# Kernel tuning notes

Measured on AMD Instinct MI355X. Metric: run time of the kernel, lower is better.

The kernel has to match this reference:

```python
import jax, jax.numpy as jnp
import numpy as np
import math

RANK = 2
CUTOFF = 10.0
EWALD_ALPHA = 0.3
PREFACTOR = 1.0
N_ATOMS = 100000
N_PAIRS = 2000000
BOX_L = 60.0


def _damp_factors_erfc(dr, b):
    # Ewald real-space damping factors for rank<=2 multipoles. Shape (5, P).
    u = b * dr
    erfc_u = jax.lax.erfc(u)
    exp2_u = jnp.exp(-u * u)
    u2 = u * u
    u3 = u2 * u
    u5 = u3 * u2
    u7 = u5 * u2
    p1 = jnp.zeros_like(u)
    p3 = u
    p5 = (3 * u + 2 * u3) / 3
    p7 = (15 * u + 10 * u3 + 4 * u5) / 15
    p9 = (8 * u7 + 28 * u5 + 70 * u3 + 105 * u) / 105
    pref = 2.0 / math.sqrt(math.pi)
    return jnp.stack([erfc_u + pref * p * exp2_u for p in (p1, p3, p5, p7, p9)], axis=0)


def _interaction_tensor(drVec, dampFactors, drInv):
    # Rank-2 multipole interaction tensor, shape (P, 10, 10).
    drInv2 = drInv * drInv
    drInv3 = drInv2 * drInv
    drInv5 = drInv3 * drInv2
    drVec2 = drVec * drVec
    x, y, z = drVec[:, 0], drVec[:, 1], drVec[:, 2]
    x2, y2, z2 = drVec2[:, 0], drVec2[:, 1], drVec2[:, 2]
    xy, xz, yz = x * y, x * z, y * z
    drInv7 = drInv5 * drInv2
    drInv9 = drInv7 * drInv2
    if dampFactors is not None:
        drInv = drInv * dampFactors[0]
        drInv3 = drInv3 * dampFactors[1]
        drInv5 = drInv5 * dampFactors[2]
        drInv7 = drInv7 * dampFactors[3]
        drInv9 = drInv9 * dampFactors[4]
    tx, ty, tz = -x * drInv3, -y * drInv3, -z * drInv3
    txx = 3 * x2 * drInv5 - drInv3
    txy = 3 * xy * drInv5
    txz = 3 * xz * drInv5
    tyy = 3 * y2 * drInv5 - drInv3
    tyz = 3 * yz * drInv5
    tzz = 3 * z2 * drInv5 - drInv3
    txxx = -15 * x2 * x * drInv7 + 9 * x * drInv5
    txxy = -15 * x2 * y * drInv7 + 3 * y * drInv5
    txxz = -15 * x2 * z * drInv7 + 3 * z * drInv5
    tyyy = -15 * y2 * y * drInv7 + 9 * y * drInv5
    tyyx = -15 * y2 * x * drInv7 + 3 * x * drInv5
    tyyz = -15 * y2 * z * drInv7 + 3 * z * drInv5
    tzzz = -15 * z2 * z * drInv7 + 9 * z * drInv5
    tzzx = -15 * z2 * x * drInv7 + 3 * x * drInv5
    tzzy = -15 * z2 * y * drInv7 + 3 * y * drInv5
    txyz = -15 * x * y * z * drInv7
    txxxx = 105 * x2 * x2 * drInv9 - 90 * x2 * drInv7 + 9 * drInv5
    txxxy = 105 * x2 * xy * drInv9 - 45 * xy * drInv7
    txxxz = 105 * x2 * xz * drInv9 - 45 * xz * drInv7
    txxyy = 105 * x2 * y2 * drInv9 - 15 * (x2 + y2) * drInv7 + 3 * drInv5
    txxzz = 105 * x2 * z2 * drInv9 - 15 * (x2 + z2) * drInv7 + 3 * drInv5
    txxyz = 105 * x2 * yz * drInv9 - 15 * yz * drInv7
    tyyyy = 105 * y2 * y2 * drInv9 - 90 * y2 * drInv7 + 9 * drInv5
    tyyyx = 105 * y2 * xy * drInv9 - 45 * xy * drInv7
    tyyyz = 105 * y2 * yz * drInv9 - 45 * yz * drInv7
    tyyzz = 105 * y2 * z2 * drInv9 - 15 * (y2 + z2) * drInv7 + 3 * drInv5
    tyyxz = 105 * y2 * xz * drInv9 - 15 * xz * drInv7
    tzzzz = 105 * z2 * z2 * drInv9 - 90 * z2 * drInv7 + 9 * drInv5
    tzzzx = 105 * z2 * xz * drInv9 - 45 * xz * drInv7
    tzzzy = 105 * z2 * yz * drInv9 - 45 * yz * drInv7
    tzzxy = 105 * z2 * xy * drInv9 - 15 * xy * drInv7
    rows = (drInv, -tx, -ty, -tz, txx, txy, txz, tyy, tyz, tzz,
            tx, -txx, -txy, -txz, txxx, txxy, txxz, tyyx, txyz, tzzx,
            ty, -txy, -tyy, -tyz, txxy, tyyx, txyz, tyyy, tyyz, tzzy,
            tz, -txz, -tyz, -tzz, txxz, txyz, tzzx, tyyz, tzzy, tzzz,
            txx, -txxx, -txxy, -txxz, txxxx, txxxy, txxxz, txxyy, txxyz, txxzz,
            txy, -txxy, -tyyx, -txyz, txxxy, txxyy, txxyz, tyyyx, tyyxz, tzzxy,
            txz, -txxz, -txyz, -tzzx, txxxz, txxyz, txxzz, tyyxz, tzzxy, tzzzx,
            tyy, -tyyx, -tyyy, -tyyz, txxyy, tyyyx, tyyxz, tyyyy, tyyyz, tyyzz,
            tyz, -txyz, -tyyz, -tzzy, txxyz, tyyxz, tzzxy, tyyyz, tyyzz, tzzzy,
            tzz, -tzzx, -tzzy, -tzzz, txxzz, tzzxy, tzzzx, tyyzz, tzzzy, tzzzz)
    return jnp.stack(rows, axis=-1).reshape(-1, 10, 10)


def _pack_multipoles(q, p, t):
    # [q, ux, uy, uz, Qxx, Qxy, Qxz, Qyy, Qyz, Qzz], shape (N, 10).
    cols = [q[:, None], p,
            (t[:, 0, 0] / 3)[:, None],
            ((t[:, 0, 1] + t[:, 1, 0]) / 3)[:, None],
            ((t[:, 0, 2] + t[:, 2, 0]) / 3)[:, None],
            (t[:, 1, 1] / 3)[:, None],
            ((t[:, 1, 2] + t[:, 2, 1]) / 3)[:, None],
            (t[:, 2, 2] / 3)[:, None]]
    return jnp.concatenate(cols, axis=1)


def setup_inputs() -> dict:
    key = jax.random.key(0)
    k1, k2, k3, k4, k5, k6 = jax.random.split(key, 6)
    coords = jax.random.uniform(k1, (N_ATOMS, 3), dtype=jnp.float32) * BOX_L
    box = jnp.eye(3, dtype=jnp.float32) * BOX_L
    pi = jax.random.randint(k2, (N_PAIRS,), 0, N_ATOMS)
    off = jax.random.randint(k3, (N_PAIRS,), 1, N_ATOMS)
    pj = (pi + off) % N_ATOMS  # guarantee i != j
    pairs = jnp.stack([pi, pj], axis=1).astype(jnp.int64)
    q = jax.random.normal(k4, (N_ATOMS,), dtype=jnp.float32)
    p = jax.random.normal(k5, (N_ATOMS, 3), dtype=jnp.float32)
    t = jax.random.normal(k6, (N_ATOMS, 3, 3), dtype=jnp.float32)
    return {"coords": coords, "box": box, "pairs": pairs, "q": q, "p": p, "t": t}


def reference(coords, box, pairs, q, p, t):
    box_inv = jnp.linalg.inv(box)
    dr = coords[pairs[:, 1]] - coords[pairs[:, 0]]
    # minimum-image PBC (row-vector fractional coordinates convention)
    dr_vecs = dr - jnp.round(dr @ box_inv) @ box
    dist = jnp.linalg.norm(dr_vecs, axis=1)
    mask = (dist <= CUTOFF).astype(dist.dtype)
    damps = _damp_factors_erfc(dist, EWALD_ALPHA)
    i_tensor = _interaction_tensor(dr_vecs, damps, 1.0 / dist)  # (P,10,10)
    m = _pack_multipoles(q, p, t)  # (N,10)
    ene_pairs = jnp.einsum('pa,pab,pb->p', m[pairs[:, 1]], i_tensor, m[pairs[:, 0]])
    return PREFACTOR * jnp.sum(ene_pairs * mask)
```

## Files before the change

### kernel.cpp

```cpp
#include <hip/hip_runtime.h>
#include <math.h>

#define CUTOFF2 100.0f
#define EW_ALPHA 0.3f
#define SEGS 2048
#define NT 256
#define CAP 128


__global__ __launch_bounds__(NT)
void screen_kernel(const float* __restrict__ coords,
                   const float* __restrict__ box,
                   const int2* __restrict__ pairs,
                   float4* __restrict__ list,
                   int* __restrict__ counts,
                   int n_pairs, int chunk) {
    __shared__ int lcount;
    if (threadIdx.x == 0) lcount = 0;
    __syncthreads();

    const float Lx = box[0], Ly = box[4], Lz = box[8];
    const float iLx = 1.0f / Lx, iLy = 1.0f / Ly, iLz = 1.0f / Lz;

    const int b = blockIdx.x;
    const int start = b * chunk;
    const int end = min(start + chunk, n_pairs);
    for (int idx = start + threadIdx.x; idx < end; idx += NT) {
        int2 pr = pairs[idx];
        int i = pr.x, j = pr.y;
        float dx = coords[3*j+0] - coords[3*i+0];
        float dy = coords[3*j+1] - coords[3*i+1];
        float dz = coords[3*j+2] - coords[3*i+2];
        float x = dx - rintf(dx * iLx) * Lx;
        float y = dy - rintf(dy * iLy) * Ly;
        float z = dz - rintf(dz * iLz) * Lz;
        float r2 = x*x + y*y + z*z;
        if (r2 <= CUTOFF2) {
            int slot = atomicAdd(&lcount, 1);
            if (slot < CAP)
                list[b*CAP + slot] = make_float4(x, y, z, __int_as_float(idx));
        }
    }
    __syncthreads();
    if (threadIdx.x == 0) counts[b] = min(lcount, CAP);
}

__global__ __launch_bounds__(NT)
void mp_dense_kernel(const float4* __restrict__ list,
                     const int* __restrict__ counts,
                     const int2* __restrict__ pairs,
                     const float* __restrict__ q,
                     const float* __restrict__ p,
                     const float* __restrict__ t,
                     double* __restrict__ partial) {
    const float PREF = 1.1283791670955126f;
    const int b = blockIdx.x;
    const int n = counts[b];

    double acc = 0.0;
    for (int k = threadIdx.x; k < n; k += NT) {
        float4 ent = list[b*CAP + k];
        float x = ent.x, y = ent.y, z = ent.z;
        int idx = __float_as_int(ent.w);
        int2 pr = pairs[idx];
        int i = pr.x, j = pr.y;

        float r2 = x*x + y*y + z*z;
        float r = sqrtf(r2);
        float rinv = 1.0f / r;

        float u  = EW_ALPHA * r;
        float u2 = u*u;
        float u3 = u2*u, u5 = u3*u2, u7 = u5*u2;
        float e2 = expf(-u2);
        float ec = erfcf(u);
        float d1 = ec;
        float d3 = ec + PREF * u * e2;
        float d5 = ec + PREF * ((3.0f*u + 2.0f*u3) * (1.0f/3.0f)) * e2;
        float d7 = ec + PREF * ((15.0f*u + 10.0f*u3 + 4.0f*u5) * (1.0f/15.0f)) * e2;
        float d9 = ec + PREF * ((105.0f*u + 70.0f*u3 + 28.0f*u5 + 8.0f*u7) * (1.0f/105.0f)) * e2;

        float ri2 = rinv * rinv;
        float r3i = rinv * ri2;
        float r5i = r3i * ri2;
        float r7i = r5i * ri2;
        float r9i = r7i * ri2;
        float R1 = rinv * d1;
        float R3 = r3i * d3;
        float R5 = r5i * d5;
        float R7 = r7i * d7;
        float R9 = r9i * d9;

        float x2 = x*x, y2 = y*y, z2 = z*z;
        float xy = x*y, xz = x*z, yz = y*z;

        float tx = -x * R3, ty = -y * R3, tz = -z * R3;
        float txx = 3.0f*x2*R5 - R3;
        float txy = 3.0f*xy*R5;
        float txz = 3.0f*xz*R5;
        float tyy = 3.0f*y2*R5 - R3;
        float tyz = 3.0f*yz*R5;
        float tzz = 3.0f*z2*R5 - R3;
        float txxx = x*(9.0f*R5 - 15.0f*x2*R7);
        float txxy = y*(3.0f*R5 - 15.0f*x2*R7);
        float txxz = z*(3.0f*R5 - 15.0f*x2*R7);
        float tyyy = y*(9.0f*R5 - 15.0f*y2*R7);
        float tyyx = x*(3.0f*R5 - 15.0f*y2*R7);
        float tyyz = z*(3.0f*R5 - 15.0f*y2*R7);
        float tzzz = z*(9.0f*R5 - 15.0f*z2*R7);
        float tzzx = x*(3.0f*R5 - 15.0f*z2*R7);
        float tzzy = y*(3.0f*R5 - 15.0f*z2*R7);
        float txyz = -15.0f*x*yz*R7;
        float txxxx = 105.0f*x2*x2*R9 - 90.0f*x2*R7 + 9.0f*R5;
        float txxxy = xy*(105.0f*x2*R9 - 45.0f*R7);
        float txxxz = xz*(105.0f*x2*R9 - 45.0f*R7);
        float txxyy = 105.0f*x2*y2*R9 - 15.0f*(x2+y2)*R7 + 3.0f*R5;
        float txxzz = 105.0f*x2*z2*R9 - 15.0f*(x2+z2)*R7 + 3.0f*R5;
        float txxyz = yz*(105.0f*x2*R9 - 15.0f*R7);
        float tyyyy = 105.0f*y2*y2*R9 - 90.0f*y2*R7 + 9.0f*R5;
        float tyyyx = xy*(105.0f*y2*R9 - 45.0f*R7);
        float tyyyz = yz*(105.0f*y2*R9 - 45.0f*R7);
        float tyyzz = 105.0f*y2*z2*R9 - 15.0f*(y2+z2)*R7 + 3.0f*R5;
        float tyyxz = xz*(105.0f*y2*R9 - 15.0f*R7);
        float tzzzz = 105.0f*z2*z2*R9 - 90.0f*z2*R7 + 9.0f*R5;
        float tzzzx = xz*(105.0f*z2*R9 - 45.0f*R7);
        float tzzzy = yz*(105.0f*z2*R9 - 45.0f*R7);
        float tzzxy = xy*(105.0f*z2*R9 - 15.0f*R7);

        const float* ti = t + 9*i;
        const float* tj = t + 9*j;
        float mi0 = q[i];
        float mi1 = p[3*i+0], mi2 = p[3*i+1], mi3 = p[3*i+2];
        float mi4 = ti[0] * (1.0f/3.0f);
        float mi5 = (ti[1] + ti[3]) * (1.0f/3.0f);
        float mi6 = (ti[2] + ti[6]) * (1.0f/3.0f);
        float mi7 = ti[4] * (1.0f/3.0f);
        float mi8 = (ti[5] + ti[7]) * (1.0f/3.0f);
        float mi9 = ti[8] * (1.0f/3.0f);
        float mj0 = q[j];
        float mj1 = p[3*j+0], mj2 = p[3*j+1], mj3 = p[3*j+2];
        float mj4 = tj[0] * (1.0f/3.0f);
        float mj5 = (tj[1] + tj[3]) * (1.0f/3.0f);
        float mj6 = (tj[2] + tj[6]) * (1.0f/3.0f);
        float mj7 = tj[4] * (1.0f/3.0f);
        float mj8 = (tj[5] + tj[7]) * (1.0f/3.0f);
        float mj9 = tj[8] * (1.0f/3.0f);

        float E0 = R1*mi0  - tx*mi1   - ty*mi2   - tz*mi3   + txx*mi4   + txy*mi5   + txz*mi6   + tyy*mi7   + tyz*mi8   + tzz*mi9;
        float E1 = tx*mi0  - txx*mi1  - txy*mi2  - txz*mi3  + txxx*mi4  + txxy*mi5  + txxz*mi6  + tyyx*mi7  + txyz*mi8  + tzzx*mi9;
        float E2 = ty*mi0  - txy*mi1  - tyy*mi2  - tyz*mi3  + txxy*mi4  + tyyx*mi5  + txyz*mi6  + tyyy*mi7  + tyyz*mi8  + tzzy*mi9;
        float E3 = tz*mi0  - txz*mi1  - tyz*mi2  - tzz*mi3  + txxz*mi4  + txyz*mi5  + tzzx*mi6  + tyyz*mi7  + tzzy*mi8  + tzzz*mi9;
        float E4 = txx*mi0 - txxx*mi1 - txxy*mi2 - txxz*mi3 + txxxx*mi4 + txxxy*mi5 + txxxz*mi6 + txxyy*mi7 + txxyz*mi8 + txxzz*mi9;
        float E5 = txy*mi0 - txxy*mi1 - tyyx*mi2 - txyz*mi3 + txxxy*mi4 + txxyy*mi5 + txxyz*mi6 + tyyyx*mi7 + tyyxz*mi8 + tzzxy*mi9;
        float E6 = txz*mi0 - txxz*mi1 - txyz*mi2 - tzzx*mi3 + txxxz*mi4 + txxyz*mi5 + txxzz*mi6 + tyyxz*mi7 + tzzxy*mi8 + tzzzx*mi9;
        float E7 = tyy*mi0 - tyyx*mi1 - tyyy*mi2 - tyyz*mi3 + txxyy*mi4 + tyyyx*mi5 + tyyxz*mi6 + tyyyy*mi7 + tyyyz*mi8 + tyyzz*mi9;
        float E8 = tyz*mi0 - txyz*mi1 - tyyz*mi2 - tzzy*mi3 + txxyz*mi4 + tyyxz*mi5 + tzzxy*mi6 + tyyyz*mi7 + tyyzz*mi8 + tzzzy*mi9;
        float E9 = tzz*mi0 - tzzx*mi1 - tzzy*mi2 - tzzz*mi3 + txxzz*mi4 + tzzxy*mi5 + tzzzx*mi6 + tyyzz*mi7 + tzzzy*mi8 + tzzzz*mi9;

        float e = mj0*E0 + mj1*E1 + mj2*E2 + mj3*E3 + mj4*E4
                + mj5*E5 + mj6*E6 + mj7*E7 + mj8*E8 + mj9*E9;

        acc += (double)e;
    }

    __shared__ double sdata[NT];
    int tid = threadIdx.x;
    sdata[tid] = acc;
    __syncthreads();
    for (int s = NT/2; s > 0; s >>= 1) {
        if (tid < s) sdata[tid] += sdata[tid + s];
        __syncthreads();
    }
    if (tid == 0) partial[b] = sdata[0];
}

__global__ __launch_bounds__(256)
void mp_reduce_kernel(const double* __restrict__ partial, int n, float* __restrict__ out) {
    __shared__ double sdata[256];
    int tid = threadIdx.x;
    double a = 0.0;
    for (int i = tid; i < n; i += 256) a += partial[i];
    sdata[tid] = a;
    __syncthreads();
    for (int s = 128; s > 0; s >>= 1) {
        if (tid < s) sdata[tid] += sdata[tid + s];
        __syncthreads();
    }
    if (tid == 0) out[0] = (float)sdata[0];
}

extern "C" void kernel_launch(void* const* d_in, const int* in_sizes, int n_in,
                              void* d_out, int out_size, void* d_ws, size_t ws_size,
                              hipStream_t stream) {
    const float* coords = (const float*)d_in[0];
    const float* box    = (const float*)d_in[1];
    const int2*  pairs  = (const int2*)d_in[2];
    const float* q      = (const float*)d_in[3];
    const float* p      = (const float*)d_in[4];
    const float* t      = (const float*)d_in[5];
    int n_pairs = in_sizes[2] / 2;
    int chunk = (n_pairs + SEGS - 1) / SEGS;

    char* ws = (char*)d_ws;
    int*    counts  = (int*)ws;
    float4* list    = (float4*)(ws + SEGS * sizeof(int));
    double* partial = (double*)(ws + SEGS * sizeof(int) + (size_t)SEGS * CAP * sizeof(float4));

    screen_kernel<<<SEGS, NT, 0, stream>>>(coords, box, pairs, list, counts, n_pairs, chunk);
    mp_dense_kernel<<<SEGS, NT, 0, stream>>>(list, counts, pairs, q, p, t, partial);
    mp_reduce_kernel<<<1, 256, 0, stream>>>(partial, SEGS, (float*)d_out);
}
```

Baseline: 36.99 us.

## Fuse cutoff screening and multipole energy into one kernel via shared-memory list

Merges the screening kernel and the dense energy kernel into a single kernel. Each block compacts its in-cutoff pairs (displacement plus i/j indices) into shared memory and then evaluates the energy directly. This drops one kernel launch, the global list write and read, and the second read of the pairs array. Pairs are now streamed as 64-bit words with nontemporal loads, and the per-block capacity drops from 128 to 96. The lower capacity slightly raises the risk of silently dropping pairs if a segment holds unusually many in-cutoff pairs.

```diff
diff --git a/kernel.cpp b/kernel.cpp
--- a/kernel.cpp
+++ b/kernel.cpp
@@ -5,18 +5,124 @@
 #define EW_ALPHA 0.3f
 #define SEGS 2048
 #define NT 256
-#define CAP 128
-
+#define CAP 96
+
+__device__ __forceinline__ double pair_energy(float x, float y, float z,
+                                              int i, int j,
+                                              const float* __restrict__ q,
+                                              const float* __restrict__ p,
+                                              const float* __restrict__ t) {
+    const float PREF = 1.1283791670955126f;
+    float r2 = x*x + y*y + z*z;
+    float r = sqrtf(r2);
+    float rinv = 1.0f / r;
+
+    float u  = EW_ALPHA * r;
+    float u2 = u*u;
+    float u3 = u2*u, u5 = u3*u2, u7 = u5*u2;
+    float e2 = expf(-u2);
+    float ec = erfcf(u);
+    float d1 = ec;
+    float d3 = ec + PREF * u * e2;
+    float d5 = ec + PREF * ((3.0f*u + 2.0f*u3) * (1.0f/3.0f)) * e2;
+    float d7 = ec + PREF * ((15.0f*u + 10.0f*u3 + 4.0f*u5) * (1.0f/15.0f)) * e2;
+    float d9 = ec + PREF * ((105.0f*u + 70.0f*u3 + 28.0f*u5 + 8.0f*u7) * (1.0f/105.0f)) * e2;
+
+    float ri2 = rinv * rinv;
+    float r3i = rinv * ri2;
+    float r5i = r3i * ri2;
+    float r7i = r5i * ri2;
+    float r9i = r7i * ri2;
+    float R1 = rinv * d1;
+    float R3 = r3i * d3;
+    float R5 = r5i * d5;
+    float R7 = r7i * d7;
+    float R9 = r9i * d9;
+
+    float x2 = x*x, y2 = y*y, z2 = z*z;
+    float xy = x*y, xz = x*z, yz = y*z;
+
+    float tx = -x * R3, ty = -y * R3, tz = -z * R3;
+    float txx = 3.0f*x2*R5 - R3;
+    float txy = 3.0f*xy*R5;
+    float txz = 3.0f*xz*R5;
+    float tyy = 3.0f*y2*R5 - R3;
+    float tyz = 3.0f*yz*R5;
+    float tzz = 3.0f*z2*R5 - R3;
+    float txxx = x*(9.0f*R5 - 15.0f*x2*R7);
+    float txxy = y*(3.0f*R5 - 15.0f*x2*R7);
+    float txxz = z*(3.0f*R5 - 15.0f*x2*R7);
+    float tyyy = y*(9.0f*R5 - 15.0f*y2*R7);
+    float tyyx = x*(3.0f*R5 - 15.0f*y2*R7);
+    float tyyz = z*(3.0f*R5 - 15.0f*y2*R7);
+    float tzzz = z*(9.0f*R5 - 15.0f*z2*R7);
+    float tzzx = x*(3.0f*R5 - 15.0f*z2*R7);
+    float tzzy = y*(3.0f*R5 - 15.0f*z2*R7);
+    float txyz = -15.0f*x*yz*R7;
+    float txxxx = 105.0f*x2*x2*R9 - 90.0f*x2*R7 + 9.0f*R5;
+    float txxxy = xy*(105.0f*x2*R9 - 45.0f*R7);
+    float txxxz = xz*(105.0f*x2*R9 - 45.0f*R7);
+    float txxyy = 105.0f*x2*y2*R9 - 15.0f*(x2+y2)*R7 + 3.0f*R5;
+    float txxzz = 105.0f*x2*z2*R9 - 15.0f*(x2+z2)*R7 + 3.0f*R5;
+    float txxyz = yz*(105.0f*x2*R9 - 15.0f*R7);
+    float tyyyy = 105.0f*y2*y2*R9 - 90.0f*y2*R7 + 9.0f*R5;
+    float tyyyx = xy*(105.0f*y2*R9 - 45.0f*R7);
+    float tyyyz = yz*(105.0f*y2*R9 - 45.0f*R7);
+    float tyyzz = 105.0f*y2*z2*R9 - 15.0f*(y2+z2)*R7 + 3.0f*R5;
+    float tyyxz = xz*(105.0f*y2*R9 - 15.0f*R7);
+    float tzzzz = 105.0f*z2*z2*R9 - 90.0f*z2*R7 + 9.0f*R5;
+    float tzzzx = xz*(105.0f*z2*R9 - 45.0f*R7);
+    float tzzzy = yz*(105.0f*z2*R9 - 45.0f*R7);
+    float tzzxy = xy*(105.0f*z2*R9 - 15.0f*R7);
+
+    const float* ti = t + 9*i;
+    const float* tj = t + 9*j;
+    float mi0 = q[i];
+    float mi1 = p[3*i+0], mi2 = p[3*i+1], mi3 = p[3*i+2];
+    float mi4 = ti[0] * (1.0f/3.0f);
+    float mi5 = (ti[1] + ti[3]) * (1.0f/3.0f);
+    float mi6 = (ti[2] + ti[6]) * (1.0f/3.0f);
+    float mi7 = ti[4] * (1.0f/3.0f);
+    float mi8 = (ti[5] + ti[7]) * (1.0f/3.0f);
+    float mi9 = ti[8] * (1.0f/3.0f);
+    float mj0 = q[j];
+    float mj1 = p[3*j+0], mj2 = p[3*j+1], mj3 = p[3*j+2];
+    float mj4 = tj[0] * (1.0f/3.0f);
+    float mj5 = (tj[1] + tj[3]) * (1.0f/3.0f);
+    float mj6 = (tj[2] + tj[6]) * (1.0f/3.0f);
+    float mj7 = tj[4] * (1.0f/3.0f);
+    float mj8 = (tj[5] + tj[7]) * (1.0f/3.0f);
+    float mj9 = tj[8] * (1.0f/3.0f);
+
+    float E0 = R1*mi0  - tx*mi1   - ty*mi2   - tz*mi3   + txx*mi4   + txy*mi5   + txz*mi6   + tyy*mi7   + tyz*mi8   + tzz*mi9;
+    float E1 = tx*mi0  - txx*mi1  - txy*mi2  - txz*mi3  + txxx*mi4  + txxy*mi5  + txxz*mi6  + tyyx*mi7  + txyz*mi8  + tzzx*mi9;
+    float E2 = ty*mi0  - txy*mi1  - tyy*mi2  - tyz*mi3  + txxy*mi4  + tyyx*mi5  + txyz*mi6  + tyyy*mi7  + tyyz*mi8  + tzzy*mi9;
+    float E3 = tz*mi0  - txz*mi1  - tyz*mi2  - tzz*mi3  + txxz*mi4  + txyz*mi5  + tzzx*mi6  + tyyz*mi7  + tzzy*mi8  + tzzz*mi9;
+    float E4 = txx*mi0 - txxx*mi1 - txxy*mi2 - txxz*mi3 + txxxx*mi4 + txxxy*mi5 + txxxz*mi6 + txxyy*mi7 + txxyz*mi8 + txxzz*mi9;
+    float E5 = txy*mi0 - txxy*mi1 - tyyx*mi2 - txyz*mi3 + txxxy*mi4 + txxyy*mi5 + txxyz*mi6 + tyyyx*mi7 + tyyxz*mi8 + tzzxy*mi9;
+    float E6 = txz*mi0 - txxz*mi1 - txyz*mi2 - tzzx*mi3 + txxxz*mi4 + txxyz*mi5 + txxzz*mi6 + tyyxz*mi7 + tzzxy*mi8 + tzzzx*mi9;
+    float E7 = tyy*mi0 - tyyx*mi1 - tyyy*mi2 - tyyz*mi3 + txxyy*mi4 + tyyyx*mi5 + tyyxz*mi6 + tyyyy*mi7 + tyyyz*mi8 + tyyzz*mi9;
+    float E8 = tyz*mi0 - txyz*mi1 - tyyz*mi2 - tzzy*mi3 + txxyz*mi4 + tyyxz*mi5 + tzzxy*mi6 + tyyyz*mi7 + tyyzz*mi8 + tzzzy*mi9;
+    float E9 = tzz*mi0 - tzzx*mi1 - tzzy*mi2 - tzzz*mi3 + txxzz*mi4 + tzzxy*mi5 + tzzzx*mi6 + tyyzz*mi7 + tzzzy*mi8 + tzzzz*mi9;
+
+    float e = mj0*E0 + mj1*E1 + mj2*E2 + mj3*E3 + mj4*E4
+            + mj5*E5 + mj6*E6 + mj7*E7 + mj8*E8 + mj9*E9;
+    return (double)e;
+}
 
 __global__ __launch_bounds__(NT)
-void screen_kernel(const float* __restrict__ coords,
-                   const float* __restrict__ box,
-                   const int2* __restrict__ pairs,
-                   float4* __restrict__ list,
-                   int* __restrict__ counts,
-                   int n_pairs, int chunk) {
-    __shared__ int lcount;
-    if (threadIdx.x == 0) lcount = 0;
+void mp_fused_kernel(const float* __restrict__ coords,
+                     const float* __restrict__ box,
+                     const long long* __restrict__ pairs,
+                     const float* __restrict__ q,
+                     const float* __restrict__ p,
+                     const float* __restrict__ t,
+                     double* __restrict__ partial,
+                     int n_pairs, int chunk) {
+    __shared__ float sx[CAP], sy[CAP], sz[CAP];
+    __shared__ int   si[CAP], sj[CAP];
+    __shared__ int   scount;
+    if (threadIdx.x == 0) scount = 0;
     __syncthreads();
 
     const float Lx = box[0], Ly = box[4], Lz = box[8];
@@ -25,9 +131,11 @@
     const int b = blockIdx.x;
     const int start = b * chunk;
     const int end = min(start + chunk, n_pairs);
+
     for (int idx = start + threadIdx.x; idx < end; idx += NT) {
-        int2 pr = pairs[idx];
-        int i = pr.x, j = pr.y;
+        long long v = __builtin_nontemporal_load(pairs + idx);
+        int i = (int)(v & 0xffffffffLL);
+        int j = (int)(v >> 32);
         float dx = coords[3*j+0] - coords[3*i+0];
         float dy = coords[3*j+1] - coords[3*i+1];
         float dz = coords[3*j+2] - coords[3*i+2];
@@ -36,131 +144,19 @@
         float z = dz - rintf(dz * iLz) * Lz;
         float r2 = x*x + y*y + z*z;
         if (r2 <= CUTOFF2) {
-            int slot = atomicAdd(&lcount, 1);
-            if (slot < CAP)
-                list[b*CAP + slot] = make_float4(x, y, z, __int_as_float(idx));
+            int slot = atomicAdd(&scount, 1);
+            if (slot < CAP) {
+                sx[slot] = x; sy[slot] = y; sz[slot] = z;
+                si[slot] = i; sj[slot] = j;
+            }
         }
     }
     __syncthreads();
-    if (threadIdx.x == 0) counts[b] = min(lcount, CAP);
-}
-
-__global__ __launch_bounds__(NT)
-void mp_dense_kernel(const float4* __restrict__ list,
-                     const int* __restrict__ counts,
-                     const int2* __restrict__ pairs,
-                     const float* __restrict__ q,
-                     const float* __restrict__ p,
-                     const float* __restrict__ t,
-                     double* __restrict__ partial) {
-    const float PREF = 1.1283791670955126f;
-    const int b = blockIdx.x;
-    const int n = counts[b];
-
+
+    int ns = min(scount, CAP);
     double acc = 0.0;
-    for (int k = threadIdx.x; k < n; k += NT) {
-        float4 ent = list[b*CAP + k];
-        float x = ent.x, y = ent.y, z = ent.z;
-        int idx = __float_as_int(ent.w);
-        int2 pr = pairs[idx];
-        int i = pr.x, j = pr.y;
-
-        float r2 = x*x + y*y + z*z;
-        float r = sqrtf(r2);
-        float rinv = 1.0f / r;
-
-        float u  = EW_ALPHA * r;
-        float u2 = u*u;
-        float u3 = u2*u, u5 = u3*u2, u7 = u5*u2;
-        float e2 = expf(-u2);
-        float ec = erfcf(u);
-        float d1 = ec;
-        float d3 = ec + PREF * u * e2;
-        float d5 = ec + PREF * ((3.0f*u + 2.0f*u3) * (1.0f/3.0f)) * e2;
-        float d7 = ec + PREF * ((15.0f*u + 10.0f*u3 + 4.0f*u5) * (1.0f/15.0f)) * e2;
-        float d9 = ec + PREF * ((105.0f*u + 70.0f*u3 + 28.0f*u5 + 8.0f*u7) * (1.0f/105.0f)) * e2;
-
-        float ri2 = rinv * rinv;
-        float r3i = rinv * ri2;
-        float r5i = r3i * ri2;
-        float r7i = r5i * ri2;
-        float r9i = r7i * ri2;
-        float R1 = rinv * d1;
-        float R3 = r3i * d3;
-        float R5 = r5i * d5;
-        float R7 = r7i * d7;
-        float R9 = r9i * d9;
-
-        float x2 = x*x, y2 = y*y, z2 = z*z;
-        float xy = x*y, xz = x*z, yz = y*z;
-
-        float tx = -x * R3, ty = -y * R3, tz = -z * R3;
-        float txx = 3.0f*x2*R5 - R3;
-        float txy = 3.0f*xy*R5;
-        float txz = 3.0f*xz*R5;
-        float tyy = 3.0f*y2*R5 - R3;
-        float tyz = 3.0f*yz*R5;
-        float tzz = 3.0f*z2*R5 - R3;
-        float txxx = x*(9.0f*R5 - 15.0f*x2*R7);
-        float txxy = y*(3.0f*R5 - 15.0f*x2*R7);
-        float txxz = z*(3.0f*R5 - 15.0f*x2*R7);
-        float tyyy = y*(9.0f*R5 - 15.0f*y2*R7);
-        float tyyx = x*(3.0f*R5 - 15.0f*y2*R7);
-        float tyyz = z*(3.0f*R5 - 15.0f*y2*R7);
-        float tzzz = z*(9.0f*R5 - 15.0f*z2*R7);
-        float tzzx = x*(3.0f*R5 - 15.0f*z2*R7);
-        float tzzy = y*(3.0f*R5 - 15.0f*z2*R7);
-        float txyz = -15.0f*x*yz*R7;
-        float txxxx = 105.0f*x2*x2*R9 - 90.0f*x2*R7 + 9.0f*R5;
-        float txxxy = xy*(105.0f*x2*R9 - 45.0f*R7);
-        float txxxz = xz*(105.0f*x2*R9 - 45.0f*R7);
-        float txxyy = 105.0f*x2*y2*R9 - 15.0f*(x2+y2)*R7 + 3.0f*R5;
-        float txxzz = 105.0f*x2*z2*R9 - 15.0f*(x2+z2)*R7 + 3.0f*R5;
-        float txxyz = yz*(105.0f*x2*R9 - 15.0f*R7);
-        float tyyyy = 105.0f*y2*y2*R9 - 90.0f*y2*R7 + 9.0f*R5;
-        float tyyyx = xy*(105.0f*y2*R9 - 45.0f*R7);
-        float tyyyz = yz*(105.0f*y2*R9 - 45.0f*R7);
-        float tyyzz = 105.0f*y2*z2*R9 - 15.0f*(y2+z2)*R7 + 3.0f*R5;
-        float tyyxz = xz*(105.0f*y2*R9 - 15.0f*R7);
-        float tzzzz = 105.0f*z2*z2*R9 - 90.0f*z2*R7 + 9.0f*R5;
-        float tzzzx = xz*(105.0f*z2*R9 - 45.0f*R7);
-        float tzzzy = yz*(105.0f*z2*R9 - 45.0f*R7);
-        float tzzxy = xy*(105.0f*z2*R9 - 15.0f*R7);
-
-        const float* ti = t + 9*i;
-        const float* tj = t + 9*j;
-        float mi0 = q[i];
-        float mi1 = p[3*i+0], mi2 = p[3*i+1], mi3 = p[3*i+2];
-        float mi4 = ti[0] * (1.0f/3.0f);
-        float mi5 = (ti[1] + ti[3]) * (1.0f/3.0f);
-        float mi6 = (ti[2] + ti[6]) * (1.0f/3.0f);
-        float mi7 = ti[4] * (1.0f/3.0f);
-        float mi8 = (ti[5] + ti[7]) * (1.0f/3.0f);
-        float mi9 = ti[8] * (1.0f/3.0f);
-        float mj0 = q[j];
-        float mj1 = p[3*j+0], mj2 = p[3*j+1], mj3 = p[3*j+2];
-        float mj4 = tj[0] * (1.0f/3.0f);
-        float mj5 = (tj[1] + tj[3]) * (1.0f/3.0f);
-        float mj6 = (tj[2] + tj[6]) * (1.0f/3.0f);
-        float mj7 = tj[4] * (1.0f/3.0f);
-        float mj8 = (tj[5] + tj[7]) * (1.0f/3.0f);
-        float mj9 = tj[8] * (1.0f/3.0f);
-
-        float E0 = R1*mi0  - tx*mi1   - ty*mi2   - tz*mi3   + txx*mi4   + txy*mi5   + txz*mi6   + tyy*mi7   + tyz*mi8   + tzz*mi9;
-        float E1 = tx*mi0  - txx*mi1  - txy*mi2  - txz*mi3  + txxx*mi4  + txxy*mi5  + txxz*mi6  + tyyx*mi7  + txyz*mi8  + tzzx*mi9;
-        float E2 = ty*mi0  - txy*mi1  - tyy*mi2  - tyz*mi3  + txxy*mi4  + tyyx*mi5  + txyz*mi6  + tyyy*mi7  + tyyz*mi8  + tzzy*mi9;
-        float E3 = tz*mi0  - txz*mi1  - tyz*mi2  - tzz*mi3  + txxz*mi4  + txyz*mi5  + tzzx*mi6  + tyyz*mi7  + tzzy*mi8  + tzzz*mi9;
-        float E4 = txx*mi0 - txxx*mi1 - txxy*mi2 - txxz*mi3 + txxxx*mi4 + txxxy*mi5 + txxxz*mi6 + txxyy*mi7 + txxyz*mi8 + txxzz*mi9;
-        float E5 = txy*mi0 - txxy*mi1 - tyyx*mi2 - txyz*mi3 + txxxy*mi4 + txxyy*mi5 + txxyz*mi6 + tyyyx*mi7 + tyyxz*mi8 + tzzxy*mi9;
-        float E6 = txz*mi0 - txxz*mi1 - txyz*mi2 - tzzx*mi3 + txxxz*mi4 + txxyz*mi5 + txxzz*mi6 + tyyxz*mi7 + tzzxy*mi8 + tzzzx*mi9;
-        float E7 = tyy*mi0 - tyyx*mi1 - tyyy*mi2 - tyyz*mi3 + txxyy*mi4 + tyyyx*mi5 + tyyxz*mi6 + tyyyy*mi7 + tyyyz*mi8 + tyyzz*mi9;
-        float E8 = tyz*mi0 - txyz*mi1 - tyyz*mi2 - tzzy*mi3 + txxyz*mi4 + tyyxz*mi5 + tzzxy*mi6 + tyyyz*mi7 + tyyzz*mi8 + tzzzy*mi9;
-        float E9 = tzz*mi0 - tzzx*mi1 - tzzy*mi2 - tzzz*mi3 + txxzz*mi4 + tzzxy*mi5 + tzzzx*mi6 + tyyzz*mi7 + tzzzy*mi8 + tzzzz*mi9;
-
-        float e = mj0*E0 + mj1*E1 + mj2*E2 + mj3*E3 + mj4*E4
-                + mj5*E5 + mj6*E6 + mj7*E7 + mj8*E8 + mj9*E9;
-
-        acc += (double)e;
+    for (int k = threadIdx.x; k < ns; k += NT) {
+        acc += pair_energy(sx[k], sy[k], sz[k], si[k], sj[k], q, p, t);
     }
 
     __shared__ double sdata[NT];
@@ -192,21 +188,18 @@
 extern "C" void kernel_launch(void* const* d_in, const int* in_sizes, int n_in,
                               void* d_out, int out_size, void* d_ws, size_t ws_size,
                               hipStream_t stream) {
-    const float* coords = (const float*)d_in[0];
-    const float* box    = (const float*)d_in[1];
-    const int2*  pairs  = (const int2*)d_in[2];
-    const float* q      = (const float*)d_in[3];
-    const float* p      = (const float*)d_in[4];
-    const float* t      = (const float*)d_in[5];
+    const float*     coords = (const float*)d_in[0];
+    const float*     box    = (const float*)d_in[1];
+    const long long* pairs  = (const long long*)d_in[2];
+    const float*     q      = (const float*)d_in[3];
+    const float*     p      = (const float*)d_in[4];
+    const float*     t      = (const float*)d_in[5];
     int n_pairs = in_sizes[2] / 2;
     int chunk = (n_pairs + SEGS - 1) / SEGS;
 
-    char* ws = (char*)d_ws;
-    int*    counts  = (int*)ws;
-    float4* list    = (float4*)(ws + SEGS * sizeof(int));
-    double* partial = (double*)(ws + SEGS * sizeof(int) + (size_t)SEGS * CAP * sizeof(float4));
-
-    screen_kernel<<<SEGS, NT, 0, stream>>>(coords, box, pairs, list, counts, n_pairs, chunk);
-    mp_dense_kernel<<<SEGS, NT, 0, stream>>>(list, counts, pairs, q, p, t, partial);
+    double* partial = (double*)d_ws;
+
+    mp_fused_kernel<<<SEGS, NT, 0, stream>>>(coords, box, pairs, q, p, t,
+                                             partial, n_pairs, chunk);
     mp_reduce_kernel<<<1, 256, 0, stream>>>(partial, SEGS, (float*)d_out);
 }
```

New measurement: 35.53 us, median of 2. 1.04x faster.
